# Kernel optimization log

Measured on AMD Instinct MI355X. Metric: run time of the kernel, lower is better.

The kernel has to match this reference:

```python
import jax, jax.numpy as jnp
import numpy as np

INPUT_DIM = 512
OUTPUT_DIM = 32
DEGREE = 8


def setup_inputs() -> dict:
    key = jax.random.key(0)
    kx, kw = jax.random.split(key)
    x = jax.random.normal(kx, (65536, INPUT_DIM), dtype=jnp.float32)
    # xavier_normal_ on [input_dim, output_dim, degree+1]: torch treats last dims as fan;
    # fan_in = output_dim*(degree+1), fan_out = input_dim*(degree+1)
    fan_in = OUTPUT_DIM * (DEGREE + 1)
    fan_out = INPUT_DIM * (DEGREE + 1)
    std = float(np.sqrt(2.0 / (fan_in + fan_out)))
    cheby_coeffs = std * jax.random.normal(kw, (INPUT_DIM, OUTPUT_DIM, DEGREE + 1), dtype=jnp.float32)
    return {"x": x, "cheby_coeffs": cheby_coeffs}


def reference(x, cheby_coeffs):
    xt = jnp.tanh(x.reshape(-1, INPUT_DIM))
    T = [jnp.ones_like(xt), 2.0 * xt]
    for n in range(2, DEGREE + 1):
        T.append(2.0 * xt * T[n - 1] - T[n - 2])
    T = jnp.stack(T, axis=-1)  # [B, I, degree+1]
    y = jnp.einsum('bij,ioj->bo', T, cheby_coeffs)  # [B, O]
    return y
```

## Files before the change

### kernel.cpp

```cpp
#include <hip/hip_runtime.h>
#include <hip/hip_fp16.h>


typedef _Float16 half8 __attribute__((ext_vector_type(8)));
typedef __fp16  fp16x2 __attribute__((ext_vector_type(2)));
typedef float float4v __attribute__((ext_vector_type(4)));

#define N_I 512
#define N_O 32
#define N_CHUNKS 16
#define STEPS 8
#define CHUNK_F16 8192

__global__ void prep(const float* __restrict__ coeffs, _Float16* __restrict__ bsw,
                     float* __restrict__ bias) {
    if (blockIdx.x == 512) {
        int o = threadIdx.x >> 3, p = threadIdx.x & 7;
        float s = 0.f;
        for (int i = p; i < N_I; i += 8) s += coeffs[(i * 32 + o) * 9];
        for (int off = 4; off; off >>= 1) s += __shfl_down(s, off, 8);
        if (p == 0) bias[o] = s;
        return;
    }
    int id = blockIdx.x * 256 + threadIdx.x;
    int jj = id & 7;
    int L  = (id >> 3) & 63;
    int t  = (id >> 9) & 1;
    int s  = id >> 10;
    int ci = s >> 3, sl = s & 7;
    int j  = sl + 1;
    int ii = ((L >> 4) << 3) + jj;
    int i  = ci * 32 + ii;
    int o  = t * 16 + (L & 15);
    bsw[id] = (_Float16)coeffs[(i * 32 + o) * 9 + j];
}

__device__ __forceinline__ float fast_tanh(float v) {
    float e = __expf(2.0f * v);
    return __builtin_fmaf(-2.0f, __builtin_amdgcn_rcpf(e + 1.0f), 1.0f);
}

__device__ __forceinline__ half8 pack8(const float* u) {
    union { fp16x2 h[4]; half8 v; } r;
    r.h[0] = __builtin_amdgcn_cvt_pkrtz(u[0], u[1]);
    r.h[1] = __builtin_amdgcn_cvt_pkrtz(u[2], u[3]);
    r.h[2] = __builtin_amdgcn_cvt_pkrtz(u[4], u[5]);
    r.h[3] = __builtin_amdgcn_cvt_pkrtz(u[6], u[7]);
    return r.v;
}

__global__ __launch_bounds__(64) void cheby_main(
        const float* __restrict__ x, const _Float16* __restrict__ bsw,
        const float* __restrict__ bias, float* __restrict__ y) {
    const int L  = threadIdx.x;
    const int q  = L >> 4;
    const int mr = L & 15;
    const int m0 = blockIdx.x * 32;
    const float* xr0 = x + (size_t)(m0 + mr) * N_I + q * 8;
    const float* xr1 = xr0 + 16 * N_I;

    float4v xa = *(const float4v*)(xr0);
    float4v xb = *(const float4v*)(xr0 + 4);
    float4v xc = *(const float4v*)(xr1);
    float4v xd = *(const float4v*)(xr1 + 4);

    float4v acc[2][2];
#pragma unroll
    for (int a = 0; a < 2; ++a)
#pragma unroll
        for (int b = 0; b < 2; ++b)
#pragma unroll
            for (int e = 0; e < 4; ++e) acc[a][b][e] = 0.f;

    const _Float16* bc = bsw + L * 8;

    for (int ci = 0; ci < N_CHUNKS; ++ci) {
        half8 bf[STEPS][2];
#pragma unroll
        for (int s = 0; s < STEPS; ++s) {
            bf[s][0] = *(const half8*)(bc + ci * CHUNK_F16 + (s * 2 + 0) * 512);
            bf[s][1] = *(const half8*)(bc + ci * CHUNK_F16 + (s * 2 + 1) * 512);
        }

        float w0[8], w1[8], up0[8], uc0[8], up1[8], uc1[8];
#pragma unroll
        for (int e = 0; e < 4; ++e) {
            w0[e]     = 2.0f * fast_tanh(xa[e]);
            w0[e + 4] = 2.0f * fast_tanh(xb[e]);
            w1[e]     = 2.0f * fast_tanh(xc[e]);
            w1[e + 4] = 2.0f * fast_tanh(xd[e]);
        }
#pragma unroll
        for (int e = 0; e < 8; ++e) {
            up0[e] = 1.0f; uc0[e] = w0[e];
            up1[e] = 1.0f; uc1[e] = w1[e];
        }

        if (ci < N_CHUNKS - 1) {
            const int o = (ci + 1) * 32;
            xa = *(const float4v*)(xr0 + o);
            xb = *(const float4v*)(xr0 + o + 4);
            xc = *(const float4v*)(xr1 + o);
            xd = *(const float4v*)(xr1 + o + 4);
        }

#pragma unroll
        for (int s = 0; s < STEPS; ++s) {
            const half8 a0 = pack8(uc0);
            const half8 a1 = pack8(uc1);
            acc[0][0] = __builtin_amdgcn_mfma_f32_16x16x32_f16(a0, bf[s][0], acc[0][0], 0, 0, 0);
            acc[0][1] = __builtin_amdgcn_mfma_f32_16x16x32_f16(a0, bf[s][1], acc[0][1], 0, 0, 0);
            acc[1][0] = __builtin_amdgcn_mfma_f32_16x16x32_f16(a1, bf[s][0], acc[1][0], 0, 0, 0);
            acc[1][1] = __builtin_amdgcn_mfma_f32_16x16x32_f16(a1, bf[s][1], acc[1][1], 0, 0, 0);
#pragma unroll
            for (int e = 0; e < 8; ++e) {
                float n0 = __builtin_fmaf(w0[e], uc0[e], -up0[e]);
                float n1 = __builtin_fmaf(w1[e], uc1[e], -up1[e]);
                up0[e] = uc0[e]; uc0[e] = n0;
                up1[e] = uc1[e]; uc1[e] = n1;
            }
        }
    }

    const float b_n0 = bias[mr];
    const float b_n1 = bias[16 + mr];
#pragma unroll
    for (int mt = 0; mt < 2; ++mt) {
#pragma unroll
        for (int e = 0; e < 4; ++e) {
            const int r = m0 + mt * 16 + q * 4 + e;
            y[(size_t)r * N_O + mr]      = acc[mt][0][e] + b_n0;
            y[(size_t)r * N_O + 16 + mr] = acc[mt][1][e] + b_n1;
        }
    }
}

extern "C" void kernel_launch(void* const* d_in, const int* in_sizes, int n_in,
                              void* d_out, int out_size, void* d_ws, size_t ws_size,
                              hipStream_t stream) {
    const float* x      = (const float*)d_in[0];
    const float* coeffs = (const float*)d_in[1];
    float* yout = (float*)d_out;

    _Float16* bsw = (_Float16*)d_ws;
    float* bias   = (float*)((char*)d_ws + 131072 * sizeof(_Float16));

    prep<<<513, 256, 0, stream>>>(coeffs, bsw, bias);
    cheby_main<<<2048, 64, 0, stream>>>(x, bsw, bias, yout);
}
```

Baseline: 224.9 us.

## Share coefficient tiles across four waves via double-buffered LDS staging

```diff
diff --git a/kernel.cpp b/kernel.cpp
--- a/kernel.cpp
+++ b/kernel.cpp
@@ -8,9 +8,11 @@
 
 #define N_I 512
 #define N_O 32
-#define N_CHUNKS 16
+#define N_PERIODS 8
 #define STEPS 8
 #define CHUNK_F16 8192
+#define PERIOD_F16 16384
+#define PERIOD_BYTES 32768
 
 __global__ void prep(const float* __restrict__ coeffs, _Float16* __restrict__ bsw,
                      float* __restrict__ bias) {
@@ -49,20 +51,20 @@
     return r.v;
 }
 
-__global__ __launch_bounds__(64) void cheby_main(
+__global__ __launch_bounds__(256, 2) void cheby_main(
         const float* __restrict__ x, const _Float16* __restrict__ bsw,
         const float* __restrict__ bias, float* __restrict__ y) {
-    const int L  = threadIdx.x;
-    const int q  = L >> 4;
-    const int mr = L & 15;
-    const int m0 = blockIdx.x * 32;
+    __shared__ __align__(16) _Float16 bl[2][PERIOD_F16];
+
+    const int tid = threadIdx.x;
+    const int wv  = tid >> 6;
+    const int L   = tid & 63;
+    const int q   = L >> 4;
+    const int mr  = L & 15;
+    const int m0  = blockIdx.x * 128 + wv * 32;
     const float* xr0 = x + (size_t)(m0 + mr) * N_I + q * 8;
     const float* xr1 = xr0 + 16 * N_I;
-
-    float4v xa = *(const float4v*)(xr0);
-    float4v xb = *(const float4v*)(xr0 + 4);
-    float4v xc = *(const float4v*)(xr1);
-    float4v xd = *(const float4v*)(xr1 + 4);
+    const char* gB = (const char*)bsw;
 
     float4v acc[2][2];
 #pragma unroll
@@ -72,16 +74,31 @@
 #pragma unroll
             for (int e = 0; e < 4; ++e) acc[a][b][e] = 0.f;
 
-    const _Float16* bc = bsw + L * 8;
+    auto stage = [&](int p, int buf) {
+        const char* gsrc = gB + (size_t)p * PERIOD_BYTES + wv * 8192 + L * 16;
+        char* lds = (char*)&bl[buf][0] + wv * 8192;
+#pragma unroll
+        for (int it = 0; it < 8; ++it) {
+            __builtin_amdgcn_global_load_lds(
+                (const __attribute__((address_space(1))) void*)(gsrc + it * 1024),
+                (__attribute__((address_space(3))) void*)(lds + it * 1024),
+                16, 0, 0);
+        }
+    };
 
-    for (int ci = 0; ci < N_CHUNKS; ++ci) {
-        half8 bf[STEPS][2];
+    auto loadx = [&](int p, float4v* v) {
 #pragma unroll
-        for (int s = 0; s < STEPS; ++s) {
-            bf[s][0] = *(const half8*)(bc + ci * CHUNK_F16 + (s * 2 + 0) * 512);
-            bf[s][1] = *(const half8*)(bc + ci * CHUNK_F16 + (s * 2 + 1) * 512);
+        for (int c = 0; c < 2; ++c) {
+            const int o = (p * 2 + c) * 32;
+            v[c * 4 + 0] = *(const float4v*)(xr0 + o);
+            v[c * 4 + 1] = *(const float4v*)(xr0 + o + 4);
+            v[c * 4 + 2] = *(const float4v*)(xr1 + o);
+            v[c * 4 + 3] = *(const float4v*)(xr1 + o + 4);
         }
+    };
 
+    auto chunk = [&](const _Float16* bb, float4v xa, float4v xb,
+                     float4v xc, float4v xd) {
         float w0[8], w1[8], up0[8], uc0[8], up1[8], uc1[8];
 #pragma unroll
         for (int e = 0; e < 4; ++e) {
@@ -95,23 +112,16 @@
             up0[e] = 1.0f; uc0[e] = w0[e];
             up1[e] = 1.0f; uc1[e] = w1[e];
         }
-
-        if (ci < N_CHUNKS - 1) {
-            const int o = (ci + 1) * 32;
-            xa = *(const float4v*)(xr0 + o);
-            xb = *(const float4v*)(xr0 + o + 4);
-            xc = *(const float4v*)(xr1 + o);
-            xd = *(const float4v*)(xr1 + o + 4);
-        }
-
 #pragma unroll
         for (int s = 0; s < STEPS; ++s) {
             const half8 a0 = pack8(uc0);
             const half8 a1 = pack8(uc1);
-            acc[0][0] = __builtin_amdgcn_mfma_f32_16x16x32_f16(a0, bf[s][0], acc[0][0], 0, 0, 0);
-            acc[0][1] = __builtin_amdgcn_mfma_f32_16x16x32_f16(a0, bf[s][1], acc[0][1], 0, 0, 0);
-            acc[1][0] = __builtin_amdgcn_mfma_f32_16x16x32_f16(a1, bf[s][0], acc[1][0], 0, 0, 0);
-            acc[1][1] = __builtin_amdgcn_mfma_f32_16x16x32_f16(a1, bf[s][1], acc[1][1], 0, 0, 0);
+            const half8 b0 = *(const half8*)(bb + (s * 2 + 0) * 512 + L * 8);
+            const half8 b1 = *(const half8*)(bb + (s * 2 + 1) * 512 + L * 8);
+            acc[0][0] = __builtin_amdgcn_mfma_f32_16x16x32_f16(a0, b0, acc[0][0], 0, 0, 0);
+            acc[0][1] = __builtin_amdgcn_mfma_f32_16x16x32_f16(a0, b1, acc[0][1], 0, 0, 0);
+            acc[1][0] = __builtin_amdgcn_mfma_f32_16x16x32_f16(a1, b0, acc[1][0], 0, 0, 0);
+            acc[1][1] = __builtin_amdgcn_mfma_f32_16x16x32_f16(a1, b1, acc[1][1], 0, 0, 0);
 #pragma unroll
             for (int e = 0; e < 8; ++e) {
                 float n0 = __builtin_fmaf(w0[e], uc0[e], -up0[e]);
@@ -120,6 +130,24 @@
                 up1[e] = uc1[e]; uc1[e] = n1;
             }
         }
+    };
+
+    float4v cur[8], nxt[8];
+    stage(0, 0);
+    loadx(0, cur);
+    __syncthreads();
+
+    for (int p = 0; p < N_PERIODS; ++p) {
+        const int buf = p & 1;
+        if (p < N_PERIODS - 1) {
+            stage(p + 1, buf ^ 1);
+            loadx(p + 1, nxt);
+        }
+        chunk(&bl[buf][0],    cur[0], cur[1], cur[2], cur[3]);
+        chunk(&bl[buf][8192], cur[4], cur[5], cur[6], cur[7]);
+#pragma unroll
+        for (int k = 0; k < 8; ++k) cur[k] = nxt[k];
+        __syncthreads();
     }
 
     const float b_n0 = bias[mr];
@@ -146,5 +174,5 @@
     float* bias   = (float*)((char*)d_ws + 131072 * sizeof(_Float16));
 
     prep<<<513, 256, 0, stream>>>(coeffs, bsw, bias);
-    cheby_main<<<2048, 64, 0, stream>>>(x, bsw, bias, yout);
+    cheby_main<<<512, 256, 0, stream>>>(x, bsw, bias, yout);
 }
```

After: 215.5 us. 1.04x faster.
